# Performance work log

Measured on AMD Instinct MI355X. Metric: run time of the kernel, lower is better.

## Reference

```python
import jax, jax.numpy as jnp
import numpy as np

PS = 7  # patch (window) size
NH = 8  # num heads for local attention
EPS = 1e-5


def _rel_index(ps):
    # standard Swin-style relative position index over a ps x ps window
    coords = np.stack(np.meshgrid(np.arange(ps), np.arange(ps), indexing='ij'))  # (2,ps,ps)
    flat = coords.reshape(2, -1)                                # (2, ps*ps)
    rel = (flat[:, :, None] - flat[:, None, :]).transpose(1, 2, 0)  # (N,N,2)
    rel[..., 0] += ps - 1
    rel[..., 1] += ps - 1
    rel[..., 0] *= 2 * ps - 1
    return rel.sum(-1)  # (N,N) values in [0,(2ps-1)^2)

REL_IDX = jnp.asarray(_rel_index(PS))  # (49,49)


def _mha(x, qkv_w, qkv_b, proj_w, proj_b, num_heads, bias):
    # x: (Bn, N, C); weights stored (in,out)
    Bn, N, C = x.shape
    d = C // num_heads
    qkv = (x @ qkv_w + qkv_b).reshape(Bn, N, 3, num_heads, d).transpose(2, 0, 3, 1, 4)
    q, k, v = qkv[0], qkv[1], qkv[2]
    attn = jnp.einsum('bhnd,bhmd->bhnm', q, k) * (d ** -0.5)
    if bias is not None:
        attn = attn + bias
    attn = jax.nn.softmax(attn, axis=-1)
    out = jnp.einsum('bhnm,bhmd->bhnd', attn, v).transpose(0, 2, 1, 3).reshape(Bn, N, C)
    return out @ proj_w + proj_b


def setup_inputs() -> dict:
    key = jax.random.key(0)
    ks = jax.random.split(key, 8)
    B, C, H, W = 4, 256, 112, 112
    s = 0.02
    return {
        'x': jax.random.normal(ks[0], (B, C, H, W), jnp.float32),
        'norm_gamma': jnp.ones((C,), jnp.float32),
        'norm_beta': jnp.zeros((C,), jnp.float32),
        'qkv_l_w': jax.random.normal(ks[1], (C, 3 * C), jnp.float32) * s,
        'qkv_l_b': jnp.zeros((3 * C,), jnp.float32),
        'proj_l_w': jax.random.normal(ks[2], (C, C), jnp.float32) * s,
        'proj_l_b': jnp.zeros((C,), jnp.float32),
        'rpb_table': jax.random.normal(ks[3], ((2 * PS - 1) ** 2, NH), jnp.float32) * s,
        'qkv_c_w': jax.random.normal(ks[4], (PS * PS, 3 * PS * PS), jnp.float32) * s,
        'qkv_c_b': jnp.zeros((3 * PS * PS,), jnp.float32),
        'proj_c_w': jax.random.normal(ks[5], (PS * PS, PS * PS), jnp.float32) * s,
        'proj_c_b': jnp.zeros((PS * PS,), jnp.float32),
        'proj_w': jax.random.normal(ks[6], (2 * C, C), jnp.float32) * s,
    }


def reference(x, norm_gamma, norm_beta, qkv_l_w, qkv_l_b, proj_l_w, proj_l_b,
              rpb_table, qkv_c_w, qkv_c_b, proj_c_w, proj_c_b, proj_w):
    B, C, H, W = x.shape
    ps, N = PS, PS * PS
    nP = (H // ps) * (W // ps)
    shortcut = x

    # b c h w -> b h w c, then LayerNorm over C
    xt = x.transpose(0, 2, 3, 1)
    mu = xt.mean(-1, keepdims=True)
    var = xt.var(-1, keepdims=True)
    xn = (xt - mu) * jax.lax.rsqrt(var + EPS) * norm_gamma + norm_beta

    # window partition -> (B*nP, N, C)
    patches = xn.reshape(B, H // ps, ps, W // ps, ps, C)
    patches = patches.transpose(0, 1, 3, 2, 4, 5).reshape(-1, N, C)

    # local windowed attention with relative position bias
    bias = rpb_table[REL_IDX].transpose(2, 0, 1)[None]  # (1,NH,N,N)
    attn_local = _mha(patches, qkv_l_w, qkv_l_b, proj_l_w, proj_l_b, NH, bias)

    # cross-channel attention: (B*C, nP, N), dim=N, single head, no RPE
    pc = patches.reshape(B, nP, N, C).transpose(0, 3, 1, 2).reshape(B * C, nP, N)
    attn_cross = _mha(pc, qkv_c_w, qkv_c_b, proj_c_w, proj_c_b, 1, None)
    attn_cross = attn_cross.reshape(B, C, nP, N).transpose(0, 2, 3, 1).reshape(-1, N, C)

    def reverse(w):  # (B*nP, N, C) -> (B, H*W, C)
        w = w.reshape(B, H // ps, W // ps, ps, ps, C)
        return w.transpose(0, 1, 3, 2, 4, 5).reshape(B, H * W, C)

    out = jnp.concatenate([reverse(attn_local), reverse(attn_cross)], axis=-1) @ proj_w
    out = out.reshape(B, H, W, C).transpose(0, 3, 1, 2)
    return (out, shortcut)
```

## Files before the change

kernel.cpp:

```cpp
#include <hip/hip_runtime.h>
#include <hip/hip_bf16.h>


#define PS 7
#define NWIN_N 49
#define CH 256
#define HH 112
#define WW 112
#define BB 4
#define NHEAD 8
#define HD 32

static constexpr size_t ELEMS = (size_t)BB * CH * HH * WW;
static constexpr size_t SZ    = ELEMS * 2;

typedef __attribute__((ext_vector_type(8))) short short8;
typedef __attribute__((ext_vector_type(4))) float f32x4;

static __device__ __forceinline__ unsigned short bf16_bits(float v) {
    __hip_bfloat16 h = __float2bfloat16(v);
    return *reinterpret_cast<unsigned short*>(&h);
}

__global__ __launch_bounds__(256) void ln_partition_kernel(
    const float* __restrict__ x, const float* __restrict__ gamma,
    const float* __restrict__ beta, __hip_bfloat16* __restrict__ patches)
{
    int blk = blockIdx.x;
    int seg = blk % 7;
    int bh = blk / 7;
    int h = bh % HH, b = bh / HH;
    int w0 = seg * 16;
    int tid = threadIdx.x;

    __shared__ float X[256][17];
    __shared__ float mus[16], rstds[16];

    #pragma unroll
    for (int l = 0; l < 16; ++l) {
        int idx = l * 256 + tid;
        int c = idx >> 4, wl = idx & 15;
        X[c][wl] = x[((size_t)(b * CH + c) * HH + h) * WW + w0 + wl];
    }
    __syncthreads();

    if (tid < 16) {
        float s = 0.f, ss = 0.f;
        for (int c = 0; c < 256; ++c) { float v = X[c][tid]; s += v; ss += v * v; }
        float mu = s * (1.f / 256.f);
        float var = ss * (1.f / 256.f) - mu * mu;
        mus[tid] = mu;
        rstds[tid] = rsqrtf(var + 1e-5f);
    }
    __syncthreads();

    int c = tid;
    float g = gamma[c], be = beta[c];
    int hp = h / PS, r = h - hp * PS;
    #pragma unroll
    for (int wl = 0; wl < 16; ++wl) {
        int w = w0 + wl;
        int wp = w / PS, cc = w - wp * PS;
        int win = (b * 16 + hp) * 16 + wp;
        int i = r * PS + cc;
        float v = (X[c][wl] - mus[wl]) * rstds[wl] * g + be;
        patches[((size_t)win * NWIN_N + i) * CH + c] = __float2bfloat16(v);
    }
}

__global__ __launch_bounds__(256) void copy_f32_kernel(
    const float* __restrict__ x, float* __restrict__ out)
{
    size_t i = ((size_t)blockIdx.x * 256 + threadIdx.x) * 4;
    *(float4*)(out + i) = *(const float4*)(x + i);
}

__global__ __launch_bounds__(256) void prep_wt_kernel(
    const float* __restrict__ W, unsigned short* __restrict__ Wt,
    int Kreal, int N, int Kpad, int Npad)
{
    int idx = blockIdx.x * 256 + threadIdx.x;
    if (idx >= Npad * Kpad) return;
    int n = idx / Kpad, k = idx - n * Kpad;
    float v = (n < N && k < Kreal) ? W[(size_t)k * N + n] : 0.f;
    Wt[idx] = bf16_bits(v);
}

__global__ __launch_bounds__(256) void bias_prep_kernel(
    const float* __restrict__ rpb, float* __restrict__ biasb)
{
    int idx = blockIdx.x * 256 + threadIdx.x;
    int head = idx >> 12;
    int rem = idx & 4095;
    int i = rem >> 6, j = rem & 63;
    float v;
    if (j >= NWIN_N) v = -1e9f;
    else if (i >= NWIN_N) v = 0.f;
    else {
        int ri = i / 7, ci = i - ri * 7;
        int rj = j / 7, cj = j - rj * 7;
        v = rpb[((ri - rj + 6) * 13 + (ci - cj + 6)) * NHEAD + head];
    }
    biasb[idx] = v;
}

__global__ __launch_bounds__(256) void pad49_kernel(
    const unsigned short* __restrict__ src, unsigned short* __restrict__ dst)
{
    size_t idx = (size_t)blockIdx.x * 256 + threadIdx.x;
    int t = idx & 63;
    size_t m = idx >> 6;
    dst[idx] = (t < 49) ? src[m * 49 + t] : (unsigned short)0;
}

__global__ __launch_bounds__(256) void gemm_mfma_kernel(
    const __hip_bfloat16* __restrict__ A1p, const __hip_bfloat16* __restrict__ A2p,
    int K1, const unsigned short* __restrict__ Wt, const float* __restrict__ bias,
    __hip_bfloat16* __restrict__ Cb, float* __restrict__ Cf,
    int M, int N, int K, int pitchN)
{
    __shared__ __align__(16) unsigned short Alds[128][72];
    __shared__ __align__(16) unsigned short Wlds[64][72];
    const unsigned short* A1 = (const unsigned short*)A1p;
    const unsigned short* A2 = (const unsigned short*)A2p;

    const int nb = gridDim.x;
    const int ntiles = nb * gridDim.y;
    const int bid = blockIdx.y * nb + blockIdx.x;
    const int chunk = ntiles >> 3;
    const int tile = (bid & 7) * chunk + (bid >> 3);
    const int m0 = (tile / nb) * 128, n0 = (tile % nb) * 64;

    const int tid = threadIdx.x, lane = tid & 63, wave = tid >> 6;
    const int wm = wave >> 1, wn = wave & 1;
    const int lr = lane & 15, lk = lane >> 4;

    f32x4 acc[4][2];
    #pragma unroll
    for (int i = 0; i < 4; ++i)
        #pragma unroll
        for (int j = 0; j < 2; ++j) acc[i][j] = (f32x4){0.f, 0.f, 0.f, 0.f};

    for (int k0 = 0; k0 < K; k0 += 64) {
        #pragma unroll
        for (int i = 0; i < 4; ++i) {
            int s = tid + 256 * i;
            int row = s >> 3, c8 = (s & 7) * 8;
            int k = k0 + c8;
            const unsigned short* src = (k < K1)
                ? A1 + (size_t)(m0 + row) * K1 + k
                : A2 + (size_t)(m0 + row) * (K - K1) + (k - K1);
            *(short8*)&Alds[row][c8] = *(const short8*)src;
        }
        #pragma unroll
        for (int i = 0; i < 2; ++i) {
            int s = tid + 256 * i;
            int row = s >> 3, c8 = (s & 7) * 8;
            *(short8*)&Wlds[row][c8] =
                *(const short8*)(Wt + (size_t)(n0 + row) * K + k0 + c8);
        }
        __syncthreads();
        #pragma unroll
        for (int kk = 0; kk < 64; kk += 32) {
            short8 a[4], w[2];
            #pragma unroll
            for (int mi = 0; mi < 4; ++mi)
                a[mi] = *(const short8*)&Alds[wm * 64 + mi * 16 + lr][kk + lk * 8];
            #pragma unroll
            for (int nj = 0; nj < 2; ++nj)
                w[nj] = *(const short8*)&Wlds[wn * 32 + nj * 16 + lr][kk + lk * 8];
            #pragma unroll
            for (int mi = 0; mi < 4; ++mi)
                #pragma unroll
                for (int nj = 0; nj < 2; ++nj)
                    acc[mi][nj] = __builtin_amdgcn_mfma_f32_16x16x32_bf16(
                        a[mi], w[nj], acc[mi][nj], 0, 0, 0);
        }
        __syncthreads();
    }

    if (Cb) {
        if ((pitchN & 7) == 0) {
            #pragma unroll
            for (int nj = 0; nj < 2; ++nj) {
                int n = n0 + wn * 32 + nj * 16 + lr;
                float bv = (bias && n < N) ? bias[n] : 0.f;
                #pragma unroll
                for (int mi = 0; mi < 4; ++mi)
                    #pragma unroll
                    for (int r = 0; r < 4; ++r)
                        Alds[wm * 64 + mi * 16 + lk * 4 + r][wn * 32 + nj * 16 + lr] =
                            bf16_bits(acc[mi][nj][r] + bv);
            }
            __syncthreads();
            #pragma unroll
            for (int i = 0; i < 4; ++i) {
                int s = tid + 256 * i;
                int row = s >> 3, c8 = (s & 7) * 8;
                if (n0 + c8 + 8 <= pitchN)
                    *(short8*)((unsigned short*)Cb + (size_t)(m0 + row) * pitchN + n0 + c8) =
                        *(const short8*)&Alds[row][c8];
            }
        } else {
            #pragma unroll
            for (int nj = 0; nj < 2; ++nj) {
                int n = n0 + wn * 32 + nj * 16 + lr;
                if (n >= N) continue;
                float bv = bias ? bias[n] : 0.f;
                #pragma unroll
                for (int mi = 0; mi < 4; ++mi) {
                    #pragma unroll
                    for (int r = 0; r < 4; ++r) {
                        int m = m0 + wm * 64 + mi * 16 + lk * 4 + r;
                        ((unsigned short*)Cb)[(size_t)m * pitchN + n] =
                            bf16_bits(acc[mi][nj][r] + bv);
                    }
                }
            }
        }
    } else {
        #pragma unroll
        for (int mi = 0; mi < 4; ++mi) {
            #pragma unroll
            for (int r = 0; r < 4; ++r) {
                int m = m0 + wm * 64 + mi * 16 + lk * 4 + r;
                int b = m / 12544, rem = m - b * 12544;
                int p = rem / 49, t = rem - p * 49;
                int h = (p >> 4) * 7 + t / 7, w = (p & 15) * 7 + (t % 7);
                size_t ob = ((size_t)(b * 256) * HH + h) * WW + w;
                #pragma unroll
                for (int nj = 0; nj < 2; ++nj) {
                    int ch = n0 + wn * 32 + nj * 16 + lr;
                    Cf[ob + (size_t)ch * (HH * WW)] = acc[mi][nj][r];
                }
            }
        }
    }
}

__global__ __launch_bounds__(64) void local_attn_mfma_kernel(
    const __hip_bfloat16* __restrict__ qkv,
    const float* __restrict__ biasb,
    __hip_bfloat16* __restrict__ outp)
{
    __shared__ __align__(16) unsigned short VT_lds[32][72];
    __shared__ __align__(16) unsigned short P_lds[16][72];

    const int win  = blockIdx.x >> 3;
    const int head = blockIdx.x & 7;
    const int lane = threadIdx.x;
    const int lr = lane & 15, lk = lane >> 4;
    const unsigned short* q16 = (const unsigned short*)qkv;
    const size_t rowbase = (size_t)win * NWIN_N;
    const float scale = 0.17677669529663687f;

    for (int t = 0; t < 32; ++t) {
        int idx = lane + 64 * t;
        int j = idx >> 5, d = idx & 31;
        unsigned short v = 0;
        if (j < NWIN_N) v = q16[(rowbase + j) * 768 + 512 + head * HD + d];
        VT_lds[d][j] = v;
    }

    short8 kf[4], qf[4];
    #pragma unroll
    for (int jt = 0; jt < 4; ++jt) {
        int j = jt * 16 + lr;
        short8 f = *(const short8*)(q16 + (rowbase + j) * 768 + 256 + head * HD + lk * 8);
        if (j >= NWIN_N) {
            #pragma unroll
            for (int e = 0; e < 8; ++e) f[e] = 0;
        }
        kf[jt] = f;
    }
    #pragma unroll
    for (int it = 0; it < 4; ++it) {
        int i = it * 16 + lr;
        qf[it] = *(const short8*)(q16 + (rowbase + i) * 768 + head * HD + lk * 8);
    }
    __syncthreads();

    #pragma unroll
    for (int it = 0; it < 4; ++it) {
        const int i = it * 16 + lr;
        f32x4 sacc[4];
        #pragma unroll
        for (int jt = 0; jt < 4; ++jt) {
            f32x4 z = (f32x4){0.f, 0.f, 0.f, 0.f};
            sacc[jt] = __builtin_amdgcn_mfma_f32_16x16x32_bf16(kf[jt], qf[it], z, 0, 0, 0);
        }
        const float* brow = biasb + head * 4096 + i * 64;
        float sv[4][4];
        float mt = -1e30f;
        #pragma unroll
        for (int jt = 0; jt < 4; ++jt) {
            float4 bv = *(const float4*)&brow[jt * 16 + lk * 4];
            sv[jt][0] = sacc[jt][0] * scale + bv.x;
            sv[jt][1] = sacc[jt][1] * scale + bv.y;
            sv[jt][2] = sacc[jt][2] * scale + bv.z;
            sv[jt][3] = sacc[jt][3] * scale + bv.w;
            #pragma unroll
            for (int r = 0; r < 4; ++r) mt = fmaxf(mt, sv[jt][r]);
        }
        mt = fmaxf(mt, __shfl_xor(mt, 16, 64));
        mt = fmaxf(mt, __shfl_xor(mt, 32, 64));
        float psum = 0.f;
        #pragma unroll
        for (int jt = 0; jt < 4; ++jt) {
            float p0 = __expf(sv[jt][0] - mt);
            float p1 = __expf(sv[jt][1] - mt);
            float p2 = __expf(sv[jt][2] - mt);
            float p3 = __expf(sv[jt][3] - mt);
            psum += (p0 + p1) + (p2 + p3);
            uint2 wv;
            wv.x = (unsigned)bf16_bits(p0) | ((unsigned)bf16_bits(p1) << 16);
            wv.y = (unsigned)bf16_bits(p2) | ((unsigned)bf16_bits(p3) << 16);
            *(uint2*)&P_lds[lr][jt * 16 + lk * 4] = wv;
        }
        psum += __shfl_xor(psum, 16, 64);
        psum += __shfl_xor(psum, 32, 64);
        __syncthreads();

        f32x4 oacc[2];
        oacc[0] = (f32x4){0.f, 0.f, 0.f, 0.f};
        oacc[1] = (f32x4){0.f, 0.f, 0.f, 0.f};
        #pragma unroll
        for (int kst = 0; kst < 2; ++kst) {
            short8 bfv = *(const short8*)&P_lds[lr][kst * 32 + lk * 8];
            #pragma unroll
            for (int dt = 0; dt < 2; ++dt) {
                short8 af = *(const short8*)&VT_lds[dt * 16 + lr][kst * 32 + lk * 8];
                oacc[dt] = __builtin_amdgcn_mfma_f32_16x16x32_bf16(af, bfv, oacc[dt], 0, 0, 0);
            }
        }
        if (i < NWIN_N) {
            float inv = 1.f / psum;
            unsigned short* orow = (unsigned short*)outp + (rowbase + i) * CH + head * HD;
            #pragma unroll
            for (int dt = 0; dt < 2; ++dt) {
                uint2 wv;
                wv.x = (unsigned)bf16_bits(oacc[dt][0] * inv)
                     | ((unsigned)bf16_bits(oacc[dt][1] * inv) << 16);
                wv.y = (unsigned)bf16_bits(oacc[dt][2] * inv)
                     | ((unsigned)bf16_bits(oacc[dt][3] * inv) << 16);
                *(uint2*)&orow[dt * 16 + lk * 4] = wv;
            }
        }
        __syncthreads();
    }
}

__global__ __launch_bounds__(256) void cross_attn_mfma_kernel(
    const __hip_bfloat16* __restrict__ qkv,
    __hip_bfloat16* __restrict__ outp)
{
    __shared__ __align__(16) unsigned short K_lds[64][72];
    __shared__ __align__(16) unsigned short VT_lds[64][72];
    __shared__ __align__(16) unsigned short P_lds[64][72];

    const int bc = blockIdx.x;
    const size_t base = (size_t)bc * 256;
    const int tid  = threadIdx.x;
    const int lane = tid & 63;
    const int wave = tid >> 6;
    const int i0w  = wave * 64;
    const int lr   = lane & 15;
    const int lk   = lane >> 4;
    const int prow = wave * 16 + lr;

    const unsigned short* q16 = (const unsigned short*)qkv;
    const float inv7 = 1.f / 7.f;

    short8 qf[4][2];
    #pragma unroll
    for (int it = 0; it < 4; ++it) {
        const unsigned short* qrow = q16 + (base + i0w + it * 16 + lr) * 160;
        #pragma unroll
        for (int kst = 0; kst < 2; ++kst) {
            int k0 = lk * 8 + kst * 32;
            short8 f;
            #pragma unroll
            for (int e = 0; e < 8; ++e) {
                int k = k0 + e;
                f[e] = (short)((k < 49) ? qrow[k] : 0);
            }
            qf[it][kst] = f;
        }
    }

    float m_run[4], l_run[4];
    f32x4 acc_o[4][4];
    #pragma unroll
    for (int it = 0; it < 4; ++it) { m_run[it] = -1e30f; l_run[it] = 0.f; }
    #pragma unroll
    for (int dt = 0; dt < 4; ++dt)
        #pragma unroll
        for (int it = 0; it < 4; ++it) acc_o[dt][it] = (f32x4){0.f, 0.f, 0.f, 0.f};

    for (int jt4 = 0; jt4 < 4; ++jt4) {
        const int j0 = jt4 * 64;
        {
            int j = tid >> 2, sub = tid & 3;
            const unsigned short* krow = q16 + (base + j0 + j) * 160 + 49;
            #pragma unroll
            for (int e = 0; e < 16; ++e) {
                int c = sub * 16 + e;
                K_lds[j][c] = (c < 49) ? krow[c] : (unsigned short)0;
            }
            int jj = tid & 63, dg = tid >> 6;
            const unsigned short* vrow = q16 + (base + j0 + jj) * 160 + 98;
            #pragma unroll
            for (int e = 0; e < 16; ++e) {
                int d = dg * 16 + e;
                VT_lds[d][jj] = (d < 49) ? vrow[d] : (unsigned short)0;
            }
        }
        __syncthreads();

        #pragma unroll
        for (int it = 0; it < 4; ++it) {
            f32x4 sacc[4];
            #pragma unroll
            for (int jt = 0; jt < 4; ++jt) sacc[jt] = (f32x4){0.f, 0.f, 0.f, 0.f};
            #pragma unroll
            for (int kst = 0; kst < 2; ++kst) {
                #pragma unroll
                for (int jt = 0; jt < 4; ++jt) {
                    short8 af = *(const short8*)&K_lds[jt * 16 + lr][lk * 8 + kst * 32];
                    sacc[jt] = __builtin_amdgcn_mfma_f32_16x16x32_bf16(
                        af, qf[it][kst], sacc[jt], 0, 0, 0);
                }
            }
            float mt = -1e30f;
            #pragma unroll
            for (int jt = 0; jt < 4; ++jt)
                #pragma unroll
                for (int r = 0; r < 4; ++r) mt = fmaxf(mt, sacc[jt][r]);
            mt = fmaxf(mt, __shfl_xor(mt, 16, 64));
            mt = fmaxf(mt, __shfl_xor(mt, 32, 64));
            float mnew = fmaxf(m_run[it], mt * inv7);
            float corr = __expf(m_run[it] - mnew);
            m_run[it] = mnew;
            l_run[it] *= corr;
            #pragma unroll
            for (int dt = 0; dt < 4; ++dt)
                #pragma unroll
                for (int r = 0; r < 4; ++r) acc_o[dt][it][r] *= corr;

            float psum = 0.f;
            #pragma unroll
            for (int jt = 0; jt < 4; ++jt) {
                float p0 = __expf(sacc[jt][0] * inv7 - mnew);
                float p1 = __expf(sacc[jt][1] * inv7 - mnew);
                float p2 = __expf(sacc[jt][2] * inv7 - mnew);
                float p3 = __expf(sacc[jt][3] * inv7 - mnew);
                psum += (p0 + p1) + (p2 + p3);
                uint2 wv;
                wv.x = (unsigned)bf16_bits(p0) | ((unsigned)bf16_bits(p1) << 16);
                wv.y = (unsigned)bf16_bits(p2) | ((unsigned)bf16_bits(p3) << 16);
                *(uint2*)&P_lds[prow][jt * 16 + lk * 4] = wv;
            }
            psum += __shfl_xor(psum, 16, 64);
            psum += __shfl_xor(psum, 32, 64);
            l_run[it] += psum;

            #pragma unroll
            for (int kst = 0; kst < 2; ++kst) {
                short8 bfv = *(const short8*)&P_lds[prow][kst * 32 + lk * 8];
                #pragma unroll
                for (int dt = 0; dt < 4; ++dt) {
                    short8 af = *(const short8*)&VT_lds[dt * 16 + lr][kst * 32 + lk * 8];
                    acc_o[dt][it] = __builtin_amdgcn_mfma_f32_16x16x32_bf16(
                        af, bfv, acc_o[dt][it], 0, 0, 0);
                }
            }
        }
        __syncthreads();
    }

    #pragma unroll
    for (int it = 0; it < 4; ++it) {
        float inv = 1.f / l_run[it];
        unsigned short* orow = (unsigned short*)outp + (base + i0w + it * 16 + lr) * 64;
        #pragma unroll
        for (int dt = 0; dt < 4; ++dt) {
            #pragma unroll
            for (int r = 0; r < 4; ++r) {
                int d = dt * 16 + lk * 4 + r;
                orow[d] = bf16_bits(acc_o[dt][it][r] * inv);
            }
        }
    }
}

__global__ __launch_bounds__(256) void transpose_bf16_kernel(
    const __hip_bfloat16* __restrict__ src, __hip_bfloat16* __restrict__ dst,
    int R, int Cc)
{
    __shared__ __hip_bfloat16 T[64][66];
    int b = blockIdx.z;
    int r0 = blockIdx.y * 64, c0 = blockIdx.x * 64;
    const __hip_bfloat16* s = src + (size_t)b * R * Cc;
    __hip_bfloat16* d = dst + (size_t)b * R * Cc;
    int tid = threadIdx.x;
    int lr = tid >> 6, lc = tid & 63;

    #pragma unroll
    for (int l = 0; l < 16; ++l) {
        int rr = l * 4 + lr;
        T[rr][lc] = s[(size_t)(r0 + rr) * Cc + c0 + lc];
    }
    __syncthreads();
    #pragma unroll
    for (int l = 0; l < 16; ++l) {
        int cc = l * 4 + lr;
        d[(size_t)(c0 + cc) * R + r0 + lc] = T[lc][cc];
    }
}

__global__ void ws_marker_kernel(float* __restrict__ out0)
{
    if (threadIdx.x == 0) out0[0] = 777.0f;
}

extern "C" void kernel_launch(void* const* d_in, const int* in_sizes, int n_in,
                              void* d_out, int out_size, void* d_ws, size_t ws_size,
                              hipStream_t stream)
{
    const float* x        = (const float*)d_in[0];
    const float* gamma    = (const float*)d_in[1];
    const float* beta     = (const float*)d_in[2];
    const float* qkv_l_w  = (const float*)d_in[3];
    const float* qkv_l_b  = (const float*)d_in[4];
    const float* proj_l_w = (const float*)d_in[5];
    const float* proj_l_b = (const float*)d_in[6];
    const float* rpb      = (const float*)d_in[7];
    const float* qkv_c_w  = (const float*)d_in[8];
    const float* qkv_c_b  = (const float*)d_in[9];
    const float* proj_c_w = (const float*)d_in[10];
    const float* proj_c_b = (const float*)d_in[11];
    const float* proj_w   = (const float*)d_in[12];

    float* out0 = (float*)d_out;
    float* out1 = out0 + ELEMS;

    copy_f32_kernel<<<(int)(ELEMS / 1024), 256, 0, stream>>>(x, out1);

    char* ws = (char*)d_ws;
    if (ws_size < 6 * SZ) {
        ws_marker_kernel<<<1, 64, 0, stream>>>(out0);
        return;
    }

    const size_t P = SZ;
    __hip_bfloat16* localOut  = (__hip_bfloat16*)(ws + 0 * P);
    unsigned short* wt_qkv_l  = (unsigned short*)(ws + 0 * P);
    float*          biasb     = (float*)(ws + 0 * P + 0x80000);
    __hip_bfloat16* patches   = (__hip_bfloat16*)(ws + 1 * P);
    __hip_bfloat16* qkv_l     = (__hip_bfloat16*)(ws + 2 * P);
    __hip_bfloat16* attnL     = (__hip_bfloat16*)(ws + 5 * P);
    char*           G         = ws + 4 * P + 0x700000;
    unsigned short* wt_proj_l = (unsigned short*)(G + 0x000000);
    unsigned short* wt_qkv_c  = (unsigned short*)(G + 0x080000);
    unsigned short* wt_proj_c = (unsigned short*)(G + 0x100000);
    unsigned short* wt_final  = (unsigned short*)(G + 0x180000);
    __hip_bfloat16* pc_dense  = (__hip_bfloat16*)(ws + 2 * P);
    __hip_bfloat16* pc_pad    = (__hip_bfloat16*)(ws + 6 * P - (size_t)262144 * 64 * 2);
    __hip_bfloat16* qkvc      = (__hip_bfloat16*)(ws + 1 * P);
    __hip_bfloat16* crossAttn = pc_pad;
    __hip_bfloat16* crossProj = (__hip_bfloat16*)(ws + 1 * P);
    __hip_bfloat16* crossT    = (__hip_bfloat16*)(ws + 2 * P);

    prep_wt_kernel<<<768, 256, 0, stream>>>(qkv_l_w, wt_qkv_l, 256, 768, 256, 768);
    bias_prep_kernel<<<128, 256, 0, stream>>>(rpb, biasb);
    ln_partition_kernel<<<BB * HH * 7, 256, 0, stream>>>(x, gamma, beta, patches);
    gemm_mfma_kernel<<<dim3(12, 392), 256, 0, stream>>>(
        patches, nullptr, 256, wt_qkv_l, qkv_l_b, qkv_l, nullptr, 50176, 768, 256, 768);
    local_attn_mfma_kernel<<<1024 * NHEAD, 64, 0, stream>>>(qkv_l, biasb, attnL);
    prep_wt_kernel<<<256, 256, 0, stream>>>(proj_l_w, wt_proj_l, 256, 256, 256, 256);
    prep_wt_kernel<<<48, 256, 0, stream>>>(qkv_c_w, wt_qkv_c, 49, 147, 64, 192);
    prep_wt_kernel<<<16, 256, 0, stream>>>(proj_c_w, wt_proj_c, 49, 49, 64, 64);
    prep_wt_kernel<<<512, 256, 0, stream>>>(proj_w, wt_final, 512, 256, 512, 256);
    gemm_mfma_kernel<<<dim3(4, 392), 256, 0, stream>>>(
        attnL, nullptr, 256, wt_proj_l, proj_l_b, localOut, nullptr, 50176, 256, 256, 256);
    transpose_bf16_kernel<<<dim3(4, 196, BB), 256, 0, stream>>>(patches, pc_dense, 12544, 256);
    pad49_kernel<<<65536, 256, 0, stream>>>(
        (const unsigned short*)pc_dense, (unsigned short*)pc_pad);
    gemm_mfma_kernel<<<dim3(3, 2048), 256, 0, stream>>>(
        pc_pad, nullptr, 64, wt_qkv_c, qkv_c_b, qkvc, nullptr, 262144, 147, 64, 160);
    cross_attn_mfma_kernel<<<1024, 256, 0, stream>>>(qkvc, crossAttn);
    gemm_mfma_kernel<<<dim3(1, 2048), 256, 0, stream>>>(
        crossAttn, nullptr, 64, wt_proj_c, proj_c_b, crossProj, nullptr, 262144, 49, 64, 49);
    transpose_bf16_kernel<<<dim3(196, 4, BB), 256, 0, stream>>>(crossProj, crossT, 256, 12544);
    gemm_mfma_kernel<<<dim3(4, 392), 256, 0, stream>>>(
        localOut, crossT, 256, wt_final, nullptr, nullptr, out0, 50176, 256, 512, 256);
}
```

Measured before the change: 378.1 us.

## Pad cross-attention QKV layout to aligned 56-column segments for vector loads

Reorders the cross-channel QKV weight and bias so Q, K and V each start at an 8-aligned column (stride 168), letting the cross-attention kernel load Q, K and V with 16-byte short8 reads instead of per-element gathers. V is staged through LDS and transposed there, P is double-buffered across row tiles, and the final output is written as packed uint2 stores. It adds two small prep kernels, a wider QKV GEMM output and an extra barrier per key tile.

```diff
diff --git a/kernel.cpp b/kernel.cpp
--- a/kernel.cpp
+++ b/kernel.cpp
@@ -84,6 +84,31 @@
     int n = idx / Kpad, k = idx - n * Kpad;
     float v = (n < N && k < Kreal) ? W[(size_t)k * N + n] : 0.f;
     Wt[idx] = bf16_bits(v);
+}
+
+__global__ __launch_bounds__(256) void prep_wt_qkvc_kernel(
+    const float* __restrict__ W, unsigned short* __restrict__ Wt)
+{
+    int idx = blockIdx.x * 256 + threadIdx.x;
+    if (idx >= 192 * 64) return;
+    int n = idx >> 6, k = idx & 63;
+    int s = -1;
+    if (n < 49) s = n;
+    else if (n >= 56 && n < 105) s = n - 7;
+    else if (n >= 112 && n < 161) s = n - 14;
+    float v = (s >= 0 && k < 49) ? W[(size_t)k * 147 + s] : 0.f;
+    Wt[idx] = bf16_bits(v);
+}
+
+__global__ __launch_bounds__(192) void prep_bias_c_kernel(
+    const float* __restrict__ b, float* __restrict__ bc)
+{
+    int n = threadIdx.x;
+    int s = -1;
+    if (n < 49) s = n;
+    else if (n >= 56 && n < 105) s = n - 7;
+    else if (n >= 112 && n < 161) s = n - 14;
+    bc[n] = (s >= 0) ? b[s] : 0.f;
 }
 
 __global__ __launch_bounds__(256) void bias_prep_kernel(
@@ -356,7 +381,7 @@
 {
     __shared__ __align__(16) unsigned short K_lds[64][72];
     __shared__ __align__(16) unsigned short VT_lds[64][72];
-    __shared__ __align__(16) unsigned short P_lds[64][72];
+    __shared__ __align__(16) unsigned short P_lds[2][64][72];
 
     const int bc = blockIdx.x;
     const size_t base = (size_t)bc * 256;
@@ -370,21 +395,16 @@
 
     const unsigned short* q16 = (const unsigned short*)qkv;
     const float inv7 = 1.f / 7.f;
+    const short8 zf = (short8){0, 0, 0, 0, 0, 0, 0, 0};
 
     short8 qf[4][2];
     #pragma unroll
     for (int it = 0; it < 4; ++it) {
-        const unsigned short* qrow = q16 + (base + i0w + it * 16 + lr) * 160;
+        const unsigned short* qrow = q16 + (base + i0w + it * 16 + lr) * 168;
         #pragma unroll
         for (int kst = 0; kst < 2; ++kst) {
             int k0 = lk * 8 + kst * 32;
-            short8 f;
-            #pragma unroll
-            for (int e = 0; e < 8; ++e) {
-                int k = k0 + e;
-                f[e] = (short)((k < 49) ? qrow[k] : 0);
-            }
-            qf[it][kst] = f;
+            qf[it][kst] = (k0 <= 48) ? *(const short8*)(qrow + k0) : zf;
         }
     }
 
@@ -400,25 +420,29 @@
     for (int jt4 = 0; jt4 < 4; ++jt4) {
         const int j0 = jt4 * 64;
         {
-            int j = tid >> 2, sub = tid & 3;
-            const unsigned short* krow = q16 + (base + j0 + j) * 160 + 49;
-            #pragma unroll
-            for (int e = 0; e < 16; ++e) {
-                int c = sub * 16 + e;
-                K_lds[j][c] = (c < 49) ? krow[c] : (unsigned short)0;
-            }
-            int jj = tid & 63, dg = tid >> 6;
-            const unsigned short* vrow = q16 + (base + j0 + jj) * 160 + 98;
+            const int jr = tid >> 3, c8 = (tid & 7) * 8;
+            #pragma unroll
+            for (int h = 0; h < 2; ++h) {
+                int jj = jr + h * 32;
+                const unsigned short* row = q16 + (base + j0 + jj) * 168;
+                *(short8*)&K_lds[jj][c8]    = (c8 <= 48) ? *(const short8*)(row + 56 + c8) : zf;
+                *(short8*)&P_lds[0][jj][c8] = (c8 <= 48) ? *(const short8*)(row + 112 + c8) : zf;
+            }
+        }
+        __syncthreads();
+        {
+            const int jj = tid & 63, dg = tid >> 6;
             #pragma unroll
             for (int e = 0; e < 16; ++e) {
                 int d = dg * 16 + e;
-                VT_lds[d][jj] = (d < 49) ? vrow[d] : (unsigned short)0;
+                VT_lds[d][jj] = P_lds[0][jj][d];
             }
         }
         __syncthreads();
 
         #pragma unroll
         for (int it = 0; it < 4; ++it) {
+            unsigned short* prowp = &P_lds[it & 1][prow][0];
             f32x4 sacc[4];
             #pragma unroll
             for (int jt = 0; jt < 4; ++jt) sacc[jt] = (f32x4){0.f, 0.f, 0.f, 0.f};
@@ -458,7 +482,7 @@
                 uint2 wv;
                 wv.x = (unsigned)bf16_bits(p0) | ((unsigned)bf16_bits(p1) << 16);
                 wv.y = (unsigned)bf16_bits(p2) | ((unsigned)bf16_bits(p3) << 16);
-                *(uint2*)&P_lds[prow][jt * 16 + lk * 4] = wv;
+                *(uint2*)(prowp + jt * 16 + lk * 4) = wv;
             }
             psum += __shfl_xor(psum, 16, 64);
             psum += __shfl_xor(psum, 32, 64);
@@ -466,7 +490,7 @@
 
             #pragma unroll
             for (int kst = 0; kst < 2; ++kst) {
-                short8 bfv = *(const short8*)&P_lds[prow][kst * 32 + lk * 8];
+                short8 bfv = *(const short8*)(prowp + kst * 32 + lk * 8);
                 #pragma unroll
                 for (int dt = 0; dt < 4; ++dt) {
                     short8 af = *(const short8*)&VT_lds[dt * 16 + lr][kst * 32 + lk * 8];
@@ -484,11 +508,12 @@
         unsigned short* orow = (unsigned short*)outp + (base + i0w + it * 16 + lr) * 64;
         #pragma unroll
         for (int dt = 0; dt < 4; ++dt) {
-            #pragma unroll
-            for (int r = 0; r < 4; ++r) {
-                int d = dt * 16 + lk * 4 + r;
-                orow[d] = bf16_bits(acc_o[dt][it][r] * inv);
-            }
+            uint2 wv;
+            wv.x = (unsigned)bf16_bits(acc_o[dt][it][0] * inv)
+                 | ((unsigned)bf16_bits(acc_o[dt][it][1] * inv) << 16);
+            wv.y = (unsigned)bf16_bits(acc_o[dt][it][2] * inv)
+                 | ((unsigned)bf16_bits(acc_o[dt][it][3] * inv) << 16);
+            *(uint2*)&orow[dt * 16 + lk * 4] = wv;
         }
     }
 }
@@ -559,11 +584,12 @@
     __hip_bfloat16* patches   = (__hip_bfloat16*)(ws + 1 * P);
     __hip_bfloat16* qkv_l     = (__hip_bfloat16*)(ws + 2 * P);
     __hip_bfloat16* attnL     = (__hip_bfloat16*)(ws + 5 * P);
-    char*           G         = ws + 4 * P + 0x700000;
+    char*           G         = ws + 4 * P + 0xB00000;
     unsigned short* wt_proj_l = (unsigned short*)(G + 0x000000);
     unsigned short* wt_qkv_c  = (unsigned short*)(G + 0x080000);
     unsigned short* wt_proj_c = (unsigned short*)(G + 0x100000);
     unsigned short* wt_final  = (unsigned short*)(G + 0x180000);
+    float*          biasc     = (float*)(G + 0x300000);
     __hip_bfloat16* pc_dense  = (__hip_bfloat16*)(ws + 2 * P);
     __hip_bfloat16* pc_pad    = (__hip_bfloat16*)(ws + 6 * P - (size_t)262144 * 64 * 2);
     __hip_bfloat16* qkvc      = (__hip_bfloat16*)(ws + 1 * P);
@@ -578,7 +604,8 @@
         patches, nullptr, 256, wt_qkv_l, qkv_l_b, qkv_l, nullptr, 50176, 768, 256, 768);
     local_attn_mfma_kernel<<<1024 * NHEAD, 64, 0, stream>>>(qkv_l, biasb, attnL);
     prep_wt_kernel<<<256, 256, 0, stream>>>(proj_l_w, wt_proj_l, 256, 256, 256, 256);
-    prep_wt_kernel<<<48, 256, 0, stream>>>(qkv_c_w, wt_qkv_c, 49, 147, 64, 192);
+    prep_wt_qkvc_kernel<<<48, 256, 0, stream>>>(qkv_c_w, wt_qkv_c);
+    prep_bias_c_kernel<<<1, 192, 0, stream>>>(qkv_c_b, biasc);
     prep_wt_kernel<<<16, 256, 0, stream>>>(proj_c_w, wt_proj_c, 49, 49, 64, 64);
     prep_wt_kernel<<<512, 256, 0, stream>>>(proj_w, wt_final, 512, 256, 512, 256);
     gemm_mfma_kernel<<<dim3(4, 392), 256, 0, stream>>>(
@@ -587,7 +614,7 @@
     pad49_kernel<<<65536, 256, 0, stream>>>(
         (const unsigned short*)pc_dense, (unsigned short*)pc_pad);
     gemm_mfma_kernel<<<dim3(3, 2048), 256, 0, stream>>>(
-        pc_pad, nullptr, 64, wt_qkv_c, qkv_c_b, qkvc, nullptr, 262144, 147, 64, 160);
+        pc_pad, nullptr, 64, wt_qkv_c, biasc, qkvc, nullptr, 262144, 161, 64, 168);
     cross_attn_mfma_kernel<<<1024, 256, 0, stream>>>(qkvc, crossAttn);
     gemm_mfma_kernel<<<dim3(1, 2048), 256, 0, stream>>>(
         crossAttn, nullptr, 64, wt_proj_c, proj_c_b, crossProj, nullptr, 262144, 49, 64, 49);
```

After: 357.4 us. 1.06x faster.
